# Optimization experiments

Measured on AMD Instinct MI355X. Metric: run time of the kernel, lower is better.

The kernel has to match this reference:

```python
import jax, jax.numpy as jnp
import numpy as np

B = 8192
IN = 512          # inputs feature dim (input_size[2])
CTX = 256         # context_input_size
CENTER = 512      # center_size
MIN_ = IN + CTX   # module_input_size = 768
FF = 1024         # n_ff_pre_units
RNN = 1024        # n_rnn_units
OUT = 512         # output_size
O2C = 256         # output_to_center_size
TOT = OUT + O2C   # total_output_size = 768


def setup_inputs() -> dict:
    key = jax.random.key(0)
    ks = jax.random.split(key, 12)
    return {
        "inputs": jax.random.normal(ks[0], (B, 1, IN), jnp.float32),
        "center_state": jax.random.normal(ks[1], (B, 1, CENTER), jnp.float32),
        "module_state": jax.random.normal(ks[2], (B, 1, RNN), jnp.float32),
        # reading_weights: truncated normal stddev 0.1 in TF; plain normal*0.1 is fine for a math reference
        "W_read": jax.random.normal(ks[3], (CENTER, CTX), jnp.float32) * 0.1,
        "W_pre": jax.random.normal(ks[4], (MIN_, FF), jnp.float32) * (1.0 / np.sqrt(MIN_)),
        "b_pre": jnp.zeros((FF,), jnp.float32),
        "Wx": jax.random.normal(ks[5], (FF, RNN), jnp.float32) * (1.0 / np.sqrt(FF)),
        "Wh": jax.random.normal(ks[6], (RNN, RNN), jnp.float32) * (1.0 / np.sqrt(RNN)),
        "b_rnn": jnp.zeros((RNN,), jnp.float32),
        "W_post": jax.random.normal(ks[7], (RNN, TOT), jnp.float32) * (1.0 / np.sqrt(RNN)),
        "b_post": jnp.zeros((TOT,), jnp.float32),
    }


def reference(inputs, center_state, module_state, W_read, W_pre, b_pre, Wx, Wh, b_rnn, W_post, b_post):
    # tf.clip_by_norm(W, 1.0): global Frobenius norm clip
    norm = jnp.sqrt(jnp.sum(W_read * W_read))
    W_clip = W_read * (1.0 / jnp.maximum(norm, 1.0))
    # context read: [B,1,CENTER] @ [CENTER,CTX] -> [B,1,CTX]
    context = jnp.einsum("btc,cd->btd", center_state, W_clip)
    module_inputs = jnp.concatenate([inputs, context], axis=2)  # [B,1,MIN_]
    rnn_in = jax.nn.relu(jnp.einsum("btf,fg->btg", module_inputs, W_pre) + b_pre)
    # SimpleRNNCell: h' = tanh(x Wx + h Wh + b)
    h_new = jnp.tanh(jnp.einsum("btf,fg->btg", rnn_in, Wx)
                     + jnp.einsum("btf,fg->btg", module_state, Wh) + b_rnn)
    module_output = jax.nn.relu(jnp.einsum("btf,fg->btg", h_new, W_post) + b_post)
    network_output = module_output[:, :, :OUT]
    module_output_to_center = module_output[:, :, OUT:]
    return (network_output, module_output_to_center, h_new)
```

## Files before the change

### kernel.cpp

```cpp
#include <hip/hip_runtime.h>

typedef __bf16 bf16x8 __attribute__((ext_vector_type(8)));
typedef float  f32x4  __attribute__((ext_vector_type(4)));
typedef unsigned short ushort8 __attribute__((ext_vector_type(8)));

#define B_ROWS 8192
#define IN_D   512
#define CTX_D  256
#define CENTER 512
#define MIN_D  768
#define FF_D   1024
#define RNN_D  1024
#define OUT_D  512
#define O2C_D  256
#define TOT_D  768

__device__ __forceinline__ unsigned short f2bf(float f) {
    unsigned int u = __builtin_bit_cast(unsigned int, f);
    u = (u + 0x7fff + ((u >> 16) & 1)) >> 16;
    return (unsigned short)u;
}

__device__ __forceinline__ void load_lds16(const void* g, void* l) {
    __builtin_amdgcn_global_load_lds(
        (const __attribute__((address_space(1))) unsigned int*)g,
        (__attribute__((address_space(3))) unsigned int*)l, 16, 0, 0);
}

__launch_bounds__(256)
__global__ void prep_all(const float* __restrict__ Wread, float* __restrict__ partials,
                         const float* __restrict__ Wpre, const float* __restrict__ Wx,
                         const float* __restrict__ Wh,  const float* __restrict__ Wpost,
                         unsigned short* __restrict__ WpreT, unsigned short* __restrict__ WxhT,
                         unsigned short* __restrict__ WpostT, unsigned short* __restrict__ WreadT,
                         const float* __restrict__ center, const float* __restrict__ inputs,
                         const float* __restrict__ mstate,
                         unsigned short* __restrict__ csB, unsigned short* __restrict__ miB,
                         unsigned short* __restrict__ rnB) {
    const int bid = blockIdx.x;
    const int tid = threadIdx.x;
    if (bid < 128) {
        __shared__ float red[4];
        const float* p = Wread + bid * 1024 + tid * 4;
        f32x4 v = *(const f32x4*)p;
        float s = v[0]*v[0] + v[1]*v[1] + v[2]*v[2] + v[3]*v[3];
        #pragma unroll
        for (int off = 32; off > 0; off >>= 1) s += __shfl_down(s, off, 64);
        if ((tid & 63) == 0) red[tid >> 6] = s;
        __syncthreads();
        if (tid == 0) partials[bid] = red[0] + red[1] + red[2] + red[3];
        return;
    }
    if (bid < 1984) {
        int g = (bid - 128) * 256 + tid;
        const float* W; unsigned short* out; int N, ostride;
        if (g < 98304)        { W = Wpre;  out = WpreT;        N = 1024; ostride = 768;  }
        else if (g < 229376)  { g -= 98304;  W = Wx;    out = WxhT;        N = 1024; ostride = 2048; }
        else if (g < 360448)  { g -= 229376; W = Wh;    out = WxhT + 1024; N = 1024; ostride = 2048; }
        else if (g < 458752)  { g -= 360448; W = Wpost; out = WpostT;      N = 768;  ostride = 1024; }
        else                  { g -= 458752; W = Wread; out = WreadT;      N = 256;  ostride = 512;  }
        int n  = g % N;
        int kg = g / N;
        ushort8 o;
        #pragma unroll
        for (int j = 0; j < 8; ++j)
            o[j] = f2bf(W[(long)(kg * 8 + j) * N + n]);
        *(ushort8*)(out + (long)n * ostride + kg * 8) = o;
        return;
    }
    long g = (long)(bid - 1984) * 256 + tid;
    const float* src; unsigned short* dst; int logc, ostride;
    if (g < 524288)       { src = center; dst = csB;        logc = 9;  ostride = 512;  }
    else if (g < 1048576) { g -= 524288;  src = inputs; dst = miB;        logc = 9;  ostride = 768;  }
    else                  { g -= 1048576; src = mstate; dst = rnB + 1024; logc = 10; ostride = 2048; }
    long e = g * 8;
    long row = e >> logc;
    int  col = (int)(e & ((1 << logc) - 1));
    f32x4 v0 = *(const f32x4*)(src + e);
    f32x4 v1 = *(const f32x4*)(src + e + 4);
    ushort8 o;
    o[0] = f2bf(v0[0]); o[1] = f2bf(v0[1]); o[2] = f2bf(v0[2]); o[3] = f2bf(v0[3]);
    o[4] = f2bf(v1[0]); o[5] = f2bf(v1[1]); o[6] = f2bf(v1[2]); o[7] = f2bf(v1[3]);
    *(ushort8*)(dst + row * (long)ostride + col) = o;
}

template<int MODE>
__launch_bounds__(256, 2)
__global__ void gemm_bt(const unsigned short* __restrict__ A,
                        const unsigned short* __restrict__ Bt,
                        int K, const float* __restrict__ bias,
                        unsigned short* __restrict__ outB, int ldob,
                        float* __restrict__ outF, int ldof) {
    __shared__ alignas(16) unsigned short sA[128 * 32];
    __shared__ alignas(16) unsigned short sB[128 * 32];

    const int tid  = threadIdx.x;
    const int wave = tid >> 6;
    const int lane = tid & 63;
    const int bn = blockIdx.x, bm = blockIdx.y;
    const int wm = wave & 1, wn = wave >> 1;
    const int lr = lane >> 4;
    const int lc = lane & 15;

    f32x4 acc[4][4] = {};

    long aoff[2], boff[2];
    #pragma unroll
    for (int j = 0; j < 2; ++j) {
        const int c   = tid + j * 256;
        const int row = c >> 2;
        const int kg  = (c & 3) ^ (row & 3);
        aoff[j] = (long)(bm * 128 + row) * K + kg * 8;
        boff[j] = (long)(bn * 128 + row) * K + kg * 8;
    }

    const int rsw = lr ^ (lc & 3);

    for (int k0 = 0; k0 < K; k0 += 32) {
        #pragma unroll
        for (int j = 0; j < 2; ++j) {
            load_lds16(A  + aoff[j] + k0, (char*)sA + j * 4096 + wave * 1024);
            load_lds16(Bt + boff[j] + k0, (char*)sB + j * 4096 + wave * 1024);
        }
        __syncthreads();

        bf16x8 af[4], bfr[4];
        #pragma unroll
        for (int t = 0; t < 4; ++t) {
            const int ar = wm * 64 + t * 16 + lc;
            af[t]  = *(const bf16x8*)(sA + ar * 32 + ((lr ^ (ar & 3)) * 8));
            const int br = wn * 64 + t * 16 + lc;
            bfr[t] = *(const bf16x8*)(sB + br * 32 + ((lr ^ (br & 3)) * 8));
        }
        #pragma unroll
        for (int i = 0; i < 4; ++i)
            #pragma unroll
            for (int j2 = 0; j2 < 4; ++j2)
                acc[i][j2] = __builtin_amdgcn_mfma_f32_16x16x32_bf16(af[i], bfr[j2], acc[i][j2], 0, 0, 0);
        __syncthreads();
    }

    float sc = 1.f;
    if constexpr (MODE == 0) {
        float s = 0.f;
        for (int i = 0; i < 128; ++i) s += bias[i];
        sc = 1.f / fmaxf(sqrtf(s), 1.f);
    }
    #pragma unroll
    for (int tn = 0; tn < 4; ++tn) {
        const int gcol = bn * 128 + wn * 64 + tn * 16 + lc;
        float bv = 0.f;
        if constexpr (MODE != 0) bv = bias[gcol];
        #pragma unroll
        for (int tm = 0; tm < 4; ++tm) {
            const int grow0 = bm * 128 + wm * 64 + tm * 16 + lr * 4;
            #pragma unroll
            for (int r = 0; r < 4; ++r) {
                const long grow = grow0 + r;
                float v = acc[tm][tn][r];
                if constexpr (MODE == 0) v *= sc;
                else v += bv;
                if constexpr (MODE == 1 || MODE == 3) v = fmaxf(v, 0.f);
                if constexpr (MODE == 2) v = tanhf(v);
                if constexpr (MODE == 0 || MODE == 1 || MODE == 2)
                    outB[grow * (long)ldob + gcol] = f2bf(v);
                if constexpr (MODE == 2)
                    outF[grow * (long)ldof + gcol] = v;
                if constexpr (MODE == 3) {
                    if (gcol < OUT_D)
                        outF[grow * OUT_D + gcol] = v;
                    else
                        outF[(long)B_ROWS * OUT_D + grow * O2C_D + (gcol - OUT_D)] = v;
                }
            }
        }
    }
}

extern "C" void kernel_launch(void* const* d_in, const int* in_sizes, int n_in,
                              void* d_out, int out_size, void* d_ws, size_t ws_size,
                              hipStream_t stream) {
    const float* inputs = (const float*)d_in[0];
    const float* center = (const float*)d_in[1];
    const float* mstate = (const float*)d_in[2];
    const float* W_read = (const float*)d_in[3];
    const float* W_pre  = (const float*)d_in[4];
    const float* b_pre  = (const float*)d_in[5];
    const float* Wx     = (const float*)d_in[6];
    const float* Wh     = (const float*)d_in[7];
    const float* b_rnn  = (const float*)d_in[8];
    const float* W_post = (const float*)d_in[9];
    const float* b_post = (const float*)d_in[10];
    float* out = (float*)d_out;

    char* ws = (char*)d_ws;
    float* partials = (float*)ws;
    unsigned short* WreadT = (unsigned short*)(ws + 1024);
    unsigned short* WpreT  = WreadT + 256 * 512;
    unsigned short* WxhT   = WpreT  + 1024 * 768;
    unsigned short* WpostT = WxhT   + (long)1024 * 2048;
    unsigned short* csB    = WpostT + 768 * 1024;
    unsigned short* miB    = csB + (long)B_ROWS * CENTER;
    unsigned short* rnB    = miB + (long)B_ROWS * MIN_D;
    unsigned short* hB     = rnB + (long)B_ROWS * 2048;

    prep_all<<<10176, 256, 0, stream>>>(W_read, partials,
                                        W_pre, Wx, Wh, W_post,
                                        WpreT, WxhT, WpostT, WreadT,
                                        center, inputs, mstate, csB, miB, rnB);

    gemm_bt<0><<<dim3(2, 64), 256, 0, stream>>>(csB, WreadT, 512, partials,
                                                miB + 512, MIN_D, nullptr, 0);
    gemm_bt<1><<<dim3(8, 64), 256, 0, stream>>>(miB, WpreT, 768, b_pre,
                                                rnB, 2048, nullptr, 0);
    gemm_bt<2><<<dim3(8, 64), 256, 0, stream>>>(rnB, WxhT, 2048, b_rnn,
                                                hB, RNN_D,
                                                out + (long)B_ROWS * TOT_D, RNN_D);
    gemm_bt<3><<<dim3(6, 64), 256, 0, stream>>>(hB, WpostT, 1024, b_post,
                                                nullptr, 0, out, 0);
}
```

Measured before the change: 274.3 us.

## Use 128x64 tiles with BK=64, load B fragments directly from global

The GEMM tile shrinks from 128x128 to 128x64 and the K step grows from 32 to 64. Only the A tile is staged in LDS, with an 8-way XOR swizzle; each wave loads its B fragments straight from global memory into registers. The launch grid is transposed so consecutive blocks share the same weight columns, and occupancy is raised to 4 blocks per CU. This cuts LDS traffic and synchronisation per MFMA and improves latency hiding, but B reuse across waves now depends on the caches and each block does less reuse per A load.

```diff
diff --git a/kernel.cpp b/kernel.cpp
--- a/kernel.cpp
+++ b/kernel.cpp
@@ -85,58 +85,63 @@
 }
 
 template<int MODE>
-__launch_bounds__(256, 2)
+__launch_bounds__(256, 4)
 __global__ void gemm_bt(const unsigned short* __restrict__ A,
                         const unsigned short* __restrict__ Bt,
                         int K, const float* __restrict__ bias,
                         unsigned short* __restrict__ outB, int ldob,
                         float* __restrict__ outF, int ldof) {
-    __shared__ alignas(16) unsigned short sA[128 * 32];
-    __shared__ alignas(16) unsigned short sB[128 * 32];
+    __shared__ alignas(16) unsigned short sA[128 * 64];
 
     const int tid  = threadIdx.x;
     const int wave = tid >> 6;
     const int lane = tid & 63;
-    const int bn = blockIdx.x, bm = blockIdx.y;
+    const int bm = blockIdx.x, bn = blockIdx.y;
     const int wm = wave & 1, wn = wave >> 1;
     const int lr = lane >> 4;
     const int lc = lane & 15;
-
-    f32x4 acc[4][4] = {};
-
-    long aoff[2], boff[2];
+    const int sw = lc & 7;
+
+    f32x4 acc[4][2] = {};
+
+    long aoff[4];
     #pragma unroll
-    for (int j = 0; j < 2; ++j) {
+    for (int j = 0; j < 4; ++j) {
         const int c   = tid + j * 256;
-        const int row = c >> 2;
-        const int kg  = (c & 3) ^ (row & 3);
+        const int row = c >> 3;
+        const int kg  = (c & 7) ^ (row & 7);
         aoff[j] = (long)(bm * 128 + row) * K + kg * 8;
-        boff[j] = (long)(bn * 128 + row) * K + kg * 8;
-    }
-
-    const int rsw = lr ^ (lc & 3);
-
-    for (int k0 = 0; k0 < K; k0 += 32) {
-        #pragma unroll
-        for (int j = 0; j < 2; ++j) {
-            load_lds16(A  + aoff[j] + k0, (char*)sA + j * 4096 + wave * 1024);
-            load_lds16(Bt + boff[j] + k0, (char*)sB + j * 4096 + wave * 1024);
+    }
+
+    const unsigned short* bp0 = Bt + (long)(bn * 64 + wn * 32 + lc) * K + lr * 8;
+    const unsigned short* bp1 = bp0 + (long)16 * K;
+
+    for (int k0 = 0; k0 < K; k0 += 64) {
+        #pragma unroll
+        for (int j = 0; j < 4; ++j)
+            load_lds16(A + aoff[j] + k0, (char*)sA + j * 4096 + wave * 1024);
+
+        bf16x8 bfr[2][2];
+        #pragma unroll
+        for (int kh = 0; kh < 2; ++kh) {
+            bfr[kh][0] = *(const bf16x8*)(bp0 + k0 + kh * 32);
+            bfr[kh][1] = *(const bf16x8*)(bp1 + k0 + kh * 32);
         }
         __syncthreads();
 
-        bf16x8 af[4], bfr[4];
-        #pragma unroll
-        for (int t = 0; t < 4; ++t) {
-            const int ar = wm * 64 + t * 16 + lc;
-            af[t]  = *(const bf16x8*)(sA + ar * 32 + ((lr ^ (ar & 3)) * 8));
-            const int br = wn * 64 + t * 16 + lc;
-            bfr[t] = *(const bf16x8*)(sB + br * 32 + ((lr ^ (br & 3)) * 8));
+        #pragma unroll
+        for (int kh = 0; kh < 2; ++kh) {
+            const int ch = (kh * 4 + lr) ^ sw;
+            bf16x8 af[4];
+            #pragma unroll
+            for (int t = 0; t < 4; ++t)
+                af[t] = *(const bf16x8*)(sA + (wm * 64 + t * 16 + lc) * 64 + ch * 8);
+            #pragma unroll
+            for (int i = 0; i < 4; ++i)
+                #pragma unroll
+                for (int u = 0; u < 2; ++u)
+                    acc[i][u] = __builtin_amdgcn_mfma_f32_16x16x32_bf16(af[i], bfr[kh][u], acc[i][u], 0, 0, 0);
         }
-        #pragma unroll
-        for (int i = 0; i < 4; ++i)
-            #pragma unroll
-            for (int j2 = 0; j2 < 4; ++j2)
-                acc[i][j2] = __builtin_amdgcn_mfma_f32_16x16x32_bf16(af[i], bfr[j2], acc[i][j2], 0, 0, 0);
         __syncthreads();
     }
 
@@ -147,8 +152,8 @@
         sc = 1.f / fmaxf(sqrtf(s), 1.f);
     }
     #pragma unroll
-    for (int tn = 0; tn < 4; ++tn) {
-        const int gcol = bn * 128 + wn * 64 + tn * 16 + lc;
+    for (int u = 0; u < 2; ++u) {
+        const int gcol = bn * 64 + wn * 32 + u * 16 + lc;
         float bv = 0.f;
         if constexpr (MODE != 0) bv = bias[gcol];
         #pragma unroll
@@ -157,7 +162,7 @@
             #pragma unroll
             for (int r = 0; r < 4; ++r) {
                 const long grow = grow0 + r;
-                float v = acc[tm][tn][r];
+                float v = acc[tm][u][r];
                 if constexpr (MODE == 0) v *= sc;
                 else v += bv;
                 if constexpr (MODE == 1 || MODE == 3) v = fmaxf(v, 0.f);
@@ -209,13 +214,13 @@
                                         WpreT, WxhT, WpostT, WreadT,
                                         center, inputs, mstate, csB, miB, rnB);
 
-    gemm_bt<0><<<dim3(2, 64), 256, 0, stream>>>(csB, WreadT, 512, partials,
+    gemm_bt<0><<<dim3(64, 4), 256, 0, stream>>>(csB, WreadT, 512, partials,
                                                 miB + 512, MIN_D, nullptr, 0);
-    gemm_bt<1><<<dim3(8, 64), 256, 0, stream>>>(miB, WpreT, 768, b_pre,
-                                                rnB, 2048, nullptr, 0);
-    gemm_bt<2><<<dim3(8, 64), 256, 0, stream>>>(rnB, WxhT, 2048, b_rnn,
-                                                hB, RNN_D,
-                                                out + (long)B_ROWS * TOT_D, RNN_D);
-    gemm_bt<3><<<dim3(6, 64), 256, 0, stream>>>(hB, WpostT, 1024, b_post,
-                                                nullptr, 0, out, 0);
-}
+    gemm_bt<1><<<dim3(64, 16), 256, 0, stream>>>(miB, WpreT, 768, b_pre,
+                                                 rnB, 2048, nullptr, 0);
+    gemm_bt<2><<<dim3(64, 16), 256, 0, stream>>>(rnB, WxhT, 2048, b_rnn,
+                                                 hB, RNN_D,
+                                                 out + (long)B_ROWS * TOT_D, RNN_D);
+    gemm_bt<3><<<dim3(64, 12), 256, 0, stream>>>(hB, WpostT, 1024, b_post,
+                                                 nullptr, 0, out, 0);
+}
```

Measured after the change: 313.9 us. 1.14x slower.
